# Kernel tuning notes

Hardware: AMD Instinct MI355X
Metric: run time of the kernel (lower is better)

Reference implementation:

```python
import jax, jax.numpy as jnp
import numpy as np

TEMP = 34.0   # Dynamic_conv2d default temperature
EPS = 1e-5    # BatchNorm eps


def setup_inputs() -> dict:
    key = jax.random.key(0)
    ks = jax.random.split(key, 4)
    B, Cin, Cout, H, W, K = 8, 32, 16, 256, 256, 4
    hidden = int(Cin * 0.25) + 1  # attention2d hidden planes = 9
    return {
        "x": jax.random.normal(ks[0], (B, Cin, H, W), jnp.float32),
        "weight": jax.random.normal(ks[1], (K, Cout, Cin, 3, 3), jnp.float32) * 0.05,
        "bias": jnp.zeros((K, Cout), jnp.float32),
        "fc1_w": jax.random.normal(ks[2], (hidden, Cin), jnp.float32) * 0.1,
        "fc2_w": jax.random.normal(ks[3], (K, hidden), jnp.float32) * 0.1,
        "fc2_b": jnp.zeros((K,), jnp.float32),
        "bn_gamma": jnp.ones((Cout,), jnp.float32),
        "bn_beta": jnp.zeros((Cout,), jnp.float32),
        "bn_mean": jnp.zeros((Cout,), jnp.float32),
        "bn_var": jnp.ones((Cout,), jnp.float32),
    }


def reference(x, weight, bias, fc1_w, fc2_w, fc2_b, bn_gamma, bn_beta, bn_mean, bn_var):
    xu = jnp.repeat(jnp.repeat(x, 2, axis=2), 2, axis=3)  # [B, Cin, 2H, 2W]

    # 2) attention over K kernels: global avg pool -> 1x1 conv -> relu -> 1x1 conv -> softmax(logits/T)
    pooled = xu.mean(axis=(2, 3))                          # [B, Cin]
    h = jax.nn.relu(pooled @ fc1_w.T)                      # [B, hidden]
    logits = h @ fc2_w.T + fc2_b                           # [B, K]
    attn = jax.nn.softmax(logits / TEMP, axis=-1)          # [B, K]

    # 3) per-sample aggregated conv weights & bias (CondConv-style)
    agg_w = jnp.einsum('bk,koihw->boihw', attn, weight)    # [B, Cout, Cin, 3, 3]
    agg_b = attn @ bias                                    # [B, Cout]

    # 4) per-sample 3x3 conv, stride 1, padding 1 (vmap instead of grouped-conv trick)
    dn = jax.lax.conv_dimension_numbers((1,) + xu.shape[1:], agg_w.shape[1:],
                                        ('NCHW', 'OIHW', 'NCHW'))
    def conv_one(xi, wi, bi):
        y = jax.lax.conv_general_dilated(xi[None], wi, window_strides=(1, 1),
                                         padding=((1, 1), (1, 1)),
                                         dimension_numbers=dn)[0]
        return y + bi[:, None, None]
    y = jax.vmap(conv_one)(xu, agg_w, agg_b)               # [B, Cout, 2H, 2W]

    # 5) BatchNorm (inference with running stats) + ReLU
    scale = bn_gamma / jnp.sqrt(bn_var + EPS)
    shift = bn_beta - bn_mean * scale
    return jax.nn.relu(y * scale[:, None, None] + shift[:, None, None])
```

## Files before the change

### kernel.cpp

```cpp
#include <hip/hip_runtime.h>
#include <hip/hip_bf16.h>

#define B_  8
#define CIN 32
#define COUT 16
#define K_  4
#define HID 9
#define HIN 256
#define WIN 256
#define HW  (HIN * WIN)
#define HOUT 512
#define WOUT 512
#define TEMP 34.0f
#define EPS_ 1e-5f

#define SLAB 1168

typedef float f32x4 __attribute__((ext_vector_type(4)));
typedef __fp16 fp16x2 __attribute__((ext_vector_type(2)));
typedef __fp16 f16x8 __attribute__((ext_vector_type(8)));

union FragB { unsigned u[4]; f16x8 h; };

__device__ inline unsigned pk2(float a, float b) {
    union { fp16x2 f; unsigned u; } x;
    x.f = __builtin_amdgcn_cvt_pkrtz(a, b);
    return x.u;
}
__device__ inline unsigned short f16b(float v) {
    union { __fp16 h; unsigned short u; } x;
    x.h = (__fp16)v;
    return x.u;
}

__global__ __launch_bounds__(1024) void pool_kernel(const float* __restrict__ x,
                                                    float* __restrict__ pooled) {
    int bc = blockIdx.x;
    const float4* p = (const float4*)(x + (size_t)bc * HW);
    float s = 0.f;
    for (int i = threadIdx.x; i < HW / 4; i += 1024) {
        float4 v = p[i];
        s += v.x + v.y + v.z + v.w;
    }
    #pragma unroll
    for (int off = 32; off > 0; off >>= 1) s += __shfl_down(s, off);
    __shared__ float red[16];
    if ((threadIdx.x & 63) == 0) red[threadIdx.x >> 6] = s;
    __syncthreads();
    if (threadIdx.x < 16) {
        float t = red[threadIdx.x];
        t += __shfl_down(t, 8);
        t += __shfl_down(t, 4);
        t += __shfl_down(t, 2);
        t += __shfl_down(t, 1);
        if (threadIdx.x == 0) pooled[bc] = t * (1.f / HW);
    }
}

__global__ __launch_bounds__(256) void attn_weights_kernel(
    const float* __restrict__ pooled, const float* __restrict__ weight,
    const float* __restrict__ bias, const float* __restrict__ fc1_w,
    const float* __restrict__ fc2_w, const float* __restrict__ fc2_b,
    const float* __restrict__ gamma, const float* __restrict__ beta,
    const float* __restrict__ mean, const float* __restrict__ var,
    unsigned short* __restrict__ wpk16, float* __restrict__ bias_eff) {
    int b = blockIdx.x;
    __shared__ float attn[K_];
    if (threadIdx.x == 0) {
        const float* pb = pooled + b * CIN;
        float h[HID];
        for (int j = 0; j < HID; ++j) {
            float s = 0.f;
            for (int c = 0; c < CIN; ++c) s += pb[c] * fc1_w[j * CIN + c];
            h[j] = fmaxf(s, 0.f);
        }
        float lg[K_];
        float mx = -1e30f;
        for (int k = 0; k < K_; ++k) {
            float s = fc2_b[k];
            for (int j = 0; j < HID; ++j) s += h[j] * fc2_w[k * HID + j];
            lg[k] = s * (1.f / TEMP);
            mx = fmaxf(mx, lg[k]);
        }
        float den = 0.f;
        for (int k = 0; k < K_; ++k) { lg[k] = expf(lg[k] - mx); den += lg[k]; }
        for (int k = 0; k < K_; ++k) attn[k] = lg[k] / den;
    }
    __syncthreads();
    float a0 = attn[0], a1 = attn[1], a2 = attn[2], a3v = attn[3];

    for (int p = threadIdx.x; p < COUT * CIN; p += 256) {
        int o = p >> 5, i = p & 31;
        float scale = gamma[o] / sqrtf(var[o] + EPS_);
        const float* w0 = weight + ((size_t)(0 * COUT + o) * CIN + i) * 9;
        const int kstr = COUT * CIN * 9;
        float a3w[9];
        #pragma unroll
        for (int t = 0; t < 9; ++t)
            a3w[t] = scale * (a0 * w0[t] + a1 * w0[kstr + t] +
                              a2 * w0[2 * kstr + t] + a3v * w0[3 * kstr + t]);
        float tmp[2][2][3];
        #pragma unroll
        for (int kx = 0; kx < 3; ++kx) {
            tmp[0][0][kx] = a3w[0 * 3 + kx];
            tmp[0][1][kx] = a3w[1 * 3 + kx] + a3w[2 * 3 + kx];
            tmp[1][0][kx] = a3w[0 * 3 + kx] + a3w[1 * 3 + kx];
            tmp[1][1][kx] = a3w[2 * 3 + kx];
        }
        float w16[16];
        #pragma unroll
        for (int py = 0; py < 2; ++py)
            #pragma unroll
            for (int px = 0; px < 2; ++px)
                #pragma unroll
                for (int u = 0; u < 2; ++u)
                    #pragma unroll
                    for (int v = 0; v < 2; ++v) {
                        const float* t = tmp[py][u];
                        float val = (px == 0) ? (v == 0 ? t[0] : t[1] + t[2])
                                              : (v == 0 ? t[0] + t[1] : t[2]);
                        w16[(py * 2 + px) * 4 + u * 2 + v] = val;
                    }
        const int ks = i >> 3, g = (i >> 1) & 3, hf = i & 1;
        const int l = g * 16 + o;
        #pragma unroll
        for (int par = 0; par < 4; ++par)
            #pragma unroll
            for (int d = 0; d < 4; ++d)
                wpk16[(((size_t)(b * 16 + par * 4 + ks) * 64 + l) * 4 + d) * 2 +
                      hf] = f16b(w16[par * 4 + d]);
    }
    if (threadIdx.x < COUT) {
        int o = threadIdx.x;
        float scale = gamma[o] / sqrtf(var[o] + EPS_);
        float shift = beta[o] - mean[o] * scale;
        float s = a0 * bias[0 * COUT + o] + a1 * bias[1 * COUT + o] +
                  a2 * bias[2 * COUT + o] + a3v * bias[3 * COUT + o];
        bias_eff[b * COUT + o] = s * scale + shift;
    }
}

__global__ __launch_bounds__(256, 2) void conv_kernel(
    const float* __restrict__ x, const unsigned* __restrict__ wpk,
    const float* __restrict__ bias_eff, float* __restrict__ out) {
    const int tile = blockIdx.x;
    const int b = blockIdx.y;
    const int r0 = (tile >> 3) * 32, c0 = (tile & 7) * 32;
    const int tid = threadIdx.x;

    __shared__ unsigned lds32[16 * SLAB];

    const float* xb = x + (size_t)b * CIN * HW;

    for (int i2 = 0; i2 < 16; ++i2) {
        const float* p0 = xb + (size_t)(2 * i2) * HW;
        for (int e = tid; e < 34 * 34; e += 256) {
            int pr = e / 34, pc = e - pr * 34;
            int gr = r0 - 1 + pr, gc = c0 - 1 + pc;
            bool ok = ((unsigned)gr < (unsigned)HIN) &
                      ((unsigned)gc < (unsigned)WIN);
            int off = ok ? (gr * WIN + gc) : 0;
            float v0 = p0[off];
            float v1 = p0[off + HW];
            if (!ok) { v0 = 0.f; v1 = 0.f; }
            lds32[i2 * SLAB + e] = pk2(v0, v1);
        }
    }
    __syncthreads();

    const int w = tid >> 6, lane = tid & 63;
    const int g = lane >> 4, n = lane & 15;

    f16x8 areg[4][4];
    {
        const f16x8* wp = (const f16x8*)wpk + (size_t)b * 1024 + lane;
        #pragma unroll
        for (int par = 0; par < 4; ++par)
            #pragma unroll
            for (int ks = 0; ks < 4; ++ks)
                areg[par][ks] = wp[(par * 4 + ks) * 64];
    }
    float bias4[4];
    #pragma unroll
    for (int q = 0; q < 4; ++q) bias4[q] = bias_eff[b * COUT + g * 4 + q];

    for (int h = 0; h < 2; ++h) {
        f32x4 acc[8][4];
        #pragma unroll
        for (int r8 = 0; r8 < 8; ++r8)
            #pragma unroll
            for (int par = 0; par < 4; ++par)
                acc[r8][par] = (f32x4){0.f, 0.f, 0.f, 0.f};

        #pragma unroll
        for (int ks = 0; ks < 4; ++ks) {
            const int base = (ks * 4 + g) * SLAB + (w * 8) * 34 + (h << 4) + n;
            unsigned nb[10][3];
            #pragma unroll
            for (int rr = 0; rr < 10; ++rr)
                #pragma unroll
                for (int dv = 0; dv < 3; ++dv)
                    nb[rr][dv] = lds32[base + rr * 34 + dv];
            #pragma unroll
            for (int r8 = 0; r8 < 8; ++r8)
                #pragma unroll
                for (int par = 0; par < 4; ++par) {
                    const int py = par >> 1, px = par & 1;
                    FragB bf;
                    bf.u[0] = nb[r8 + py][px];
                    bf.u[1] = nb[r8 + py][px + 1];
                    bf.u[2] = nb[r8 + py + 1][px];
                    bf.u[3] = nb[r8 + py + 1][px + 1];
                    acc[r8][par] = __builtin_amdgcn_mfma_f32_16x16x32_f16(
                        areg[par][ks], bf.h, acc[r8][par], 0, 0, 0);
                }
        }

        #pragma unroll
        for (int r8 = 0; r8 < 8; ++r8) {
            const int rloc = w * 8 + r8;
            #pragma unroll
            for (int py = 0; py < 2; ++py) {
                const int y = 2 * (r0 + rloc) + py;
                #pragma unroll
                for (int q = 0; q < 4; ++q) {
                    float2 st;
                    st.x = fmaxf(acc[r8][2 * py + 0][q] + bias4[q], 0.f);
                    st.y = fmaxf(acc[r8][2 * py + 1][q] + bias4[q], 0.f);
                    *(float2*)&out[((size_t)(b * COUT + g * 4 + q) * HOUT + y) *
                                       WOUT +
                                   2 * (c0 + (h << 4) + n)] = st;
                }
            }
        }
    }
}

extern "C" void kernel_launch(void* const* d_in, const int* in_sizes, int n_in,
                              void* d_out, int out_size, void* d_ws, size_t ws_size,
                              hipStream_t stream) {
    const float* x      = (const float*)d_in[0];
    const float* weight = (const float*)d_in[1];
    const float* bias   = (const float*)d_in[2];
    const float* fc1_w  = (const float*)d_in[3];
    const float* fc2_w  = (const float*)d_in[4];
    const float* fc2_b  = (const float*)d_in[5];
    const float* bn_g   = (const float*)d_in[6];
    const float* bn_b   = (const float*)d_in[7];
    const float* bn_m   = (const float*)d_in[8];
    const float* bn_v   = (const float*)d_in[9];
    float* out = (float*)d_out;

    float* ws = (float*)d_ws;
    float*    pooled   = ws;
    float*    bias_eff = ws + 256;
    unsigned* wpk      = (unsigned*)(ws + 512);

    pool_kernel<<<dim3(B_ * CIN), dim3(1024), 0, stream>>>(x, pooled);
    attn_weights_kernel<<<dim3(B_), dim3(256), 0, stream>>>(
        pooled, weight, bias, fc1_w, fc2_w, fc2_b, bn_g, bn_b, bn_m, bn_v,
        (unsigned short*)wpk, bias_eff);
    conv_kernel<<<dim3(64, B_), dim3(256), 0, stream>>>(
        x, wpk, bias_eff, out);
}
```

Baseline: 97.32 us.

## Halve conv tile height, shrink accumulators, and hoist weight loads before staging

The conv tile drops from 32 to 16 input rows, so the grid doubles to 128x8 blocks and the LDS slab shrinks. Each wave now processes two 2-row chunks with a small 2x4 accumulator set instead of eight rows at once. This cuts register and LDS pressure, allowing more resident blocks and better latency hiding. The weight fragment loads move ahead of the LDS staging loop so they overlap with it. In exchange, halo overhead rises because 18 rows are staged for every 16 computed instead of 34 for 32.

New measurement: 115.6 us. 18.7% more time.

```diff
diff --git a/kernel.cpp b/kernel.cpp
--- a/kernel.cpp
+++ b/kernel.cpp
@@ -14,7 +14,8 @@
 #define TEMP 34.0f
 #define EPS_ 1e-5f
 
-#define SLAB 1168
+#define SROWS 18
+#define SLAB  624
 
 typedef float f32x4 __attribute__((ext_vector_type(4)));
 typedef __fp16 fp16x2 __attribute__((ext_vector_type(2)));
@@ -140,21 +141,34 @@
     }
 }
 
-__global__ __launch_bounds__(256, 2) void conv_kernel(
+__global__ __launch_bounds__(256) void conv_kernel(
     const float* __restrict__ x, const unsigned* __restrict__ wpk,
     const float* __restrict__ bias_eff, float* __restrict__ out) {
     const int tile = blockIdx.x;
     const int b = blockIdx.y;
-    const int r0 = (tile >> 3) * 32, c0 = (tile & 7) * 32;
+    const int r0 = (tile >> 3) * 16, c0 = (tile & 7) * 32;
     const int tid = threadIdx.x;
 
     __shared__ unsigned lds32[16 * SLAB];
+
+    const int w = tid >> 6, lane = tid & 63;
+    const int g = lane >> 4, n = lane & 15;
+
+    f16x8 areg[4][4];
+    {
+        const f16x8* wp = (const f16x8*)wpk + (size_t)b * 1024 + lane;
+        #pragma unroll
+        for (int par = 0; par < 4; ++par)
+            #pragma unroll
+            for (int ks = 0; ks < 4; ++ks)
+                areg[par][ks] = wp[(par * 4 + ks) * 64];
+    }
 
     const float* xb = x + (size_t)b * CIN * HW;
 
     for (int i2 = 0; i2 < 16; ++i2) {
         const float* p0 = xb + (size_t)(2 * i2) * HW;
-        for (int e = tid; e < 34 * 34; e += 256) {
+        for (int e = tid; e < SROWS * 34; e += 256) {
             int pr = e / 34, pc = e - pr * 34;
             int gr = r0 - 1 + pr, gc = c0 - 1 + pc;
             bool ok = ((unsigned)gr < (unsigned)HIN) &
@@ -168,68 +182,60 @@
     }
     __syncthreads();
 
-    const int w = tid >> 6, lane = tid & 63;
-    const int g = lane >> 4, n = lane & 15;
-
-    f16x8 areg[4][4];
-    {
-        const f16x8* wp = (const f16x8*)wpk + (size_t)b * 1024 + lane;
-        #pragma unroll
-        for (int par = 0; par < 4; ++par)
-            #pragma unroll
-            for (int ks = 0; ks < 4; ++ks)
-                areg[par][ks] = wp[(par * 4 + ks) * 64];
-    }
     float bias4[4];
     #pragma unroll
     for (int q = 0; q < 4; ++q) bias4[q] = bias_eff[b * COUT + g * 4 + q];
 
     for (int h = 0; h < 2; ++h) {
-        f32x4 acc[8][4];
-        #pragma unroll
-        for (int r8 = 0; r8 < 8; ++r8)
-            #pragma unroll
-            for (int par = 0; par < 4; ++par)
-                acc[r8][par] = (f32x4){0.f, 0.f, 0.f, 0.f};
-
-        #pragma unroll
-        for (int ks = 0; ks < 4; ++ks) {
-            const int base = (ks * 4 + g) * SLAB + (w * 8) * 34 + (h << 4) + n;
-            unsigned nb[10][3];
-            #pragma unroll
-            for (int rr = 0; rr < 10; ++rr)
-                #pragma unroll
-                for (int dv = 0; dv < 3; ++dv)
-                    nb[rr][dv] = lds32[base + rr * 34 + dv];
-            #pragma unroll
-            for (int r8 = 0; r8 < 8; ++r8)
-                #pragma unroll
-                for (int par = 0; par < 4; ++par) {
-                    const int py = par >> 1, px = par & 1;
-                    FragB bf;
-                    bf.u[0] = nb[r8 + py][px];
-                    bf.u[1] = nb[r8 + py][px + 1];
-                    bf.u[2] = nb[r8 + py + 1][px];
-                    bf.u[3] = nb[r8 + py + 1][px + 1];
-                    acc[r8][par] = __builtin_amdgcn_mfma_f32_16x16x32_f16(
-                        areg[par][ks], bf.h, acc[r8][par], 0, 0, 0);
-                }
-        }
-
-        #pragma unroll
-        for (int r8 = 0; r8 < 8; ++r8) {
-            const int rloc = w * 8 + r8;
-            #pragma unroll
-            for (int py = 0; py < 2; ++py) {
-                const int y = 2 * (r0 + rloc) + py;
-                #pragma unroll
-                for (int q = 0; q < 4; ++q) {
-                    float2 st;
-                    st.x = fmaxf(acc[r8][2 * py + 0][q] + bias4[q], 0.f);
-                    st.y = fmaxf(acc[r8][2 * py + 1][q] + bias4[q], 0.f);
-                    *(float2*)&out[((size_t)(b * COUT + g * 4 + q) * HOUT + y) *
-                                       WOUT +
-                                   2 * (c0 + (h << 4) + n)] = st;
+        #pragma unroll
+        for (int p2 = 0; p2 < 2; ++p2) {
+            const int rA = w * 4 + p2 * 2;
+
+            f32x4 acc[2][4];
+            #pragma unroll
+            for (int rr = 0; rr < 2; ++rr)
+                #pragma unroll
+                for (int par = 0; par < 4; ++par)
+                    acc[rr][par] = (f32x4){0.f, 0.f, 0.f, 0.f};
+
+            #pragma unroll
+            for (int ks = 0; ks < 4; ++ks) {
+                const int base = (ks * 4 + g) * SLAB + rA * 34 + (h << 4) + n;
+                unsigned nb[4][3];
+                #pragma unroll
+                for (int rr = 0; rr < 4; ++rr)
+                    #pragma unroll
+                    for (int dv = 0; dv < 3; ++dv)
+                        nb[rr][dv] = lds32[base + rr * 34 + dv];
+                #pragma unroll
+                for (int rr = 0; rr < 2; ++rr)
+                    #pragma unroll
+                    for (int par = 0; par < 4; ++par) {
+                        const int py = par >> 1, px = par & 1;
+                        FragB bf;
+                        bf.u[0] = nb[rr + py][px];
+                        bf.u[1] = nb[rr + py][px + 1];
+                        bf.u[2] = nb[rr + py + 1][px];
+                        bf.u[3] = nb[rr + py + 1][px + 1];
+                        acc[rr][par] = __builtin_amdgcn_mfma_f32_16x16x32_f16(
+                            areg[par][ks], bf.h, acc[rr][par], 0, 0, 0);
+                    }
+            }
+
+            #pragma unroll
+            for (int rr = 0; rr < 2; ++rr) {
+                #pragma unroll
+                for (int py = 0; py < 2; ++py) {
+                    const int y = 2 * (r0 + rA + rr) + py;
+                    #pragma unroll
+                    for (int q = 0; q < 4; ++q) {
+                        float2 st;
+                        st.x = fmaxf(acc[rr][2 * py + 0][q] + bias4[q], 0.f);
+                        st.y = fmaxf(acc[rr][2 * py + 1][q] + bias4[q], 0.f);
+                        *(float2*)&out[((size_t)(b * COUT + g * 4 + q) * HOUT +
+                                        y) * WOUT +
+                                       2 * (c0 + (h << 4) + n)] = st;
+                    }
                 }
             }
         }
@@ -260,6 +266,6 @@
     attn_weights_kernel<<<dim3(B_), dim3(256), 0, stream>>>(
         pooled, weight, bias, fc1_w, fc2_w, fc2_b, bn_g, bn_b, bn_m, bn_v,
         (unsigned short*)wpk, bias_eff);
-    conv_kernel<<<dim3(64, B_), dim3(256), 0, stream>>>(
+    conv_kernel<<<dim3(128, B_), dim3(256), 0, stream>>>(
         x, wpk, bias_eff, out);
 }
```
